# Kernel tuning notes

Measured on AMD Instinct MI355X. Metric: run time of the kernel, lower is better.

The kernel has to match this reference:

```python
import jax, jax.numpy as jnp
import numpy as np

N_NODES = 50000
N_EDGES = 600000
D_IN = 128
D_HID = 128
N_CLASSES = 64
BN_EPS = 1e-5


def _bn(x, gamma, beta):
    # BatchNorm1d with batch statistics (training-mode math, biased var)
    mu = jnp.mean(x, axis=0)
    var = jnp.mean((x - mu) ** 2, axis=0)
    return gamma * (x - mu) * jax.lax.rsqrt(var + BN_EPS) + beta


def _gin_layer(h, src, dst, W1, b1, g1, be1, W2, b2, g2, be2):
    n = h.shape[0]
    msgs = h[src]  # [E, D] gather (copy_src)
    s = jax.ops.segment_sum(msgs, dst, num_segments=n)
    cnt = jax.ops.segment_sum(jnp.ones((dst.shape[0],), h.dtype), dst, num_segments=n)
    neigh = s / jnp.maximum(cnt, 1.0)[:, None]  # mean over in-neighbors, 0 if none
    x = h + neigh  # (1 + eps) * h + neigh with eps = 0
    x = jax.nn.relu(_bn(x @ W1 + b1, g1, be1))
    x = jax.nn.relu(_bn(x @ W2 + b2, g2, be2))
    return x


def setup_inputs() -> dict:
    key = jax.random.key(0)
    ks = jax.random.split(key, 32)
    inp = {
        "features": jax.random.normal(ks[0], (N_NODES, D_IN), dtype=jnp.float32),
        "src": jax.random.randint(ks[1], (N_EDGES,), 0, N_NODES, dtype=jnp.int32),
        "dst": jax.random.randint(ks[2], (N_EDGES,), 0, N_NODES, dtype=jnp.int32),
    }
    dims = [(D_IN, D_HID), (D_HID, D_HID), (D_HID, N_CLASSES)]
    ki = 3
    for li, (din, dout) in enumerate(dims):
        sc1 = 1.0 / np.sqrt(din)
        sc2 = 1.0 / np.sqrt(dout)
        inp[f"W1_{li}"] = jax.random.uniform(ks[ki + 0], (din, dout), jnp.float32, -sc1, sc1)
        inp[f"b1_{li}"] = jax.random.uniform(ks[ki + 1], (dout,), jnp.float32, -sc1, sc1)
        inp[f"g1_{li}"] = jnp.ones((dout,), jnp.float32)
        inp[f"be1_{li}"] = jnp.zeros((dout,), jnp.float32)
        inp[f"W2_{li}"] = jax.random.uniform(ks[ki + 2], (dout, dout), jnp.float32, -sc2, sc2)
        inp[f"b2_{li}"] = jax.random.uniform(ks[ki + 3], (dout,), jnp.float32, -sc2, sc2)
        inp[f"g2_{li}"] = jnp.ones((dout,), jnp.float32)
        inp[f"be2_{li}"] = jnp.zeros((dout,), jnp.float32)
        ki += 4
    return inp


def reference(features, src, dst,
              W1_0, b1_0, g1_0, be1_0, W2_0, b2_0, g2_0, be2_0,
              W1_1, b1_1, g1_1, be1_1, W2_1, b2_1, g2_1, be2_1,
              W1_2, b1_2, g1_2, be1_2, W2_2, b2_2, g2_2, be2_2):
    h = features
    h = _gin_layer(h, src, dst, W1_0, b1_0, g1_0, be1_0, W2_0, b2_0, g2_0, be2_0)
    h = _gin_layer(h, src, dst, W1_1, b1_1, g1_1, be1_1, W2_1, b2_1, g2_1, be2_1)
    h = _gin_layer(h, src, dst, W1_2, b1_2, g1_2, be1_2, W2_2, b2_2, g2_2, be2_2)
    return h
```

## Files before the change

### kernel.cpp

```cpp
#include <hip/hip_runtime.h>

#define NN 50000
#define NE 600000
#define SREP 64

typedef __attribute__((ext_vector_type(8))) short short8;
typedef __attribute__((ext_vector_type(4))) float f32x4;

__device__ __forceinline__ float bf2f(unsigned short u){
  union { unsigned int i; float f; } c; c.i = ((unsigned int)u) << 16; return c.f;
}
__device__ __forceinline__ float lof(unsigned v){
  union { unsigned int i; float f; } c; c.i = v << 16; return c.f;
}
__device__ __forceinline__ float hif(unsigned v){
  union { unsigned int i; float f; } c; c.i = v & 0xFFFF0000u; return c.f;
}
__device__ __forceinline__ unsigned short f2b(float f){
  union { float f; unsigned int i; } c; c.f = f;
  unsigned int i = c.i;
  return (unsigned short)((i + 0x7FFFu + ((i >> 16) & 1u)) >> 16);
}

template<int N>
__device__ __forceinline__ void compute_ab(const float* __restrict__ st,
    const float* __restrict__ gam, const float* __restrict__ bet, float2* absh){
  int tid = threadIdx.x;
  if (tid < N){
    float s = 0.f, q = 0.f;
    #pragma unroll 16
    for (int r = 0; r < SREP; ++r){
      s += st[r*2*N + tid];
      q += st[r*2*N + N + tid];
    }
    float mu = s * (1.f/(float)NN);
    float var = fmaxf(q * (1.f/(float)NN) - mu*mu, 0.f);
    float a = gam[tid] * rsqrtf(var + 1e-5f);
    absh[tid] = make_float2(a, bet[tid] - mu*a);
  }
}

struct W6 { const float* w[6]; unsigned short* o[6]; };
__global__ __launch_bounds__(256) void k_pre(const float* __restrict__ features,
    unsigned short* __restrict__ H0, unsigned short* __restrict__ Hp,
    const int* __restrict__ dst, int* __restrict__ deg, W6 jb){
  int b = blockIdx.x, tid = threadIdx.x;
  if (b < 6250){
    int i = b*256 + tid;
    float4 v = ((const float4*)features)[i];
    uint2 o;
    o.x = (unsigned)f2b(v.x) | ((unsigned)f2b(v.y) << 16);
    o.y = (unsigned)f2b(v.z) | ((unsigned)f2b(v.w) << 16);
    ((uint2*)H0)[i] = o;
  } else if (b < 6250 + 2344){
    int i = (b - 6250)*256 + tid;
    if (i < NE) atomicAdd(&deg[dst[i]], 1);
  } else if (b < 6250 + 2344 + 304){
    int i = (b - 8594)*256 + tid;
    if (i < 77824){
      int job, base, K, N;
      if (i < 65536){ job = i >> 14; base = job << 14; K = 128; N = 128; }
      else if (i < 73728){ job = 4; base = 65536; K = 128; N = 64; }
      else { job = 5; base = 73728; K = 64; N = 64; }
      int t = i - base;
      int k = t & (K-1);
      int n = t / K;
      jb.o[job][t] = f2b(jb.w[job][k*N + n]);
    }
  } else {
    if (tid < 32){
      unsigned short* bp = (tid < 16) ? H0 : Hp;
      ((uint4*)bp)[(size_t)NN*16 + (tid & 15)] = make_uint4(0,0,0,0);
    }
  }
}

__global__ void k_offsets(const int* __restrict__ deg, int* __restrict__ row_off,
                          int* __restrict__ cur, int* __restrict__ col,
                          int* __restrict__ total){
  __shared__ int ws[4];
  __shared__ int wbase[4];
  int tid = threadIdx.x, lane = tid & 63, wid = tid >> 6;
  int i = blockIdx.x*256 + tid;
  int v = (i < NN) ? deg[i] : 0;
  int vp = (v + 3) & ~3;
  int x = vp;
  #pragma unroll
  for (int o = 1; o < 64; o <<= 1){
    int t = __shfl_up(x, o);
    if (lane >= o) x += t;
  }
  if (lane == 63) ws[wid] = x;
  __syncthreads();
  if (tid == 0){
    int s0 = ws[0], s1 = ws[1], s2 = ws[2], s3 = ws[3];
    int b = atomicAdd(total, s0+s1+s2+s3);
    wbase[0] = b; wbase[1] = b+s0; wbase[2] = b+s0+s1; wbase[3] = b+s0+s1+s2;
  }
  __syncthreads();
  if (i < NN){
    int excl = wbase[wid] + x - vp;
    row_off[i] = excl;
    cur[i] = excl;
    for (int t = v; t < vp; ++t) col[excl + t] = NN;
  }
}

__global__ void k_fill(const int* __restrict__ src, const int* __restrict__ dst,
                       int* __restrict__ cur, int* __restrict__ col, int e){
  int i = blockIdx.x*blockDim.x + threadIdx.x;
  if (i >= e) return;
  int d = dst[i];
  int pos = atomicAdd(&cur[d], 1);
  col[pos] = src[i];
}

__global__ __launch_bounds__(256) void k_agg(const unsigned short* __restrict__ H,
    const int* __restrict__ row_off, const int* __restrict__ deg,
    const int* __restrict__ col, unsigned short* __restrict__ X){
  int tid = threadIdx.x;
  int lane = tid & 63, wave = tid >> 6;
  int p = lane & 15, q = lane >> 4;
  const uint4* hp4 = (const uint4*)H;
  int node = (blockIdx.x*4 + wave)*4 + q;
  int beg = row_off[node];
  int d = deg[node];
  int dp = (d + 3) & ~3;
  int m = dp;
  m = max(m, __shfl_xor(m, 16));
  m = max(m, __shfl_xor(m, 32));
  uint4 hv = hp4[(size_t)node*16 + p];
  float s[8];
  #pragma unroll
  for (int e = 0; e < 8; ++e) s[e] = 0.f;
  auto ACC = [&](uint4 v){
    s[0] += lof(v.x); s[1] += hif(v.x);
    s[2] += lof(v.y); s[3] += hif(v.y);
    s[4] += lof(v.z); s[5] += hif(v.z);
    s[6] += lof(v.w); s[7] += hif(v.w);
  };
  for (int e0 = 0; e0 < m; e0 += 8){
    int idx[8];
    #pragma unroll
    for (int u = 0; u < 8; ++u){
      int e = e0 + u;
      int cv = col[beg + e];
      idx[u] = (e < dp) ? cv : NN;
    }
    uint4 vv[8];
    #pragma unroll
    for (int u = 0; u < 8; ++u) vv[u] = hp4[(size_t)idx[u]*16 + p];
    #pragma unroll
    for (int u = 0; u < 8; ++u) ACC(vv[u]);
  }
  float inv = 1.f / (float)(d > 0 ? d : 1);
  float h[8] = {lof(hv.x),hif(hv.x),lof(hv.y),hif(hv.y),
                lof(hv.z),hif(hv.z),lof(hv.w),hif(hv.w)};
  unsigned w[4];
  #pragma unroll
  for (int u = 0; u < 4; ++u){
    float x0 = h[2*u]   + s[2*u]*inv;
    float x1 = h[2*u+1] + s[2*u+1]*inv;
    w[u] = (unsigned)f2b(x0) | ((unsigned)f2b(x1) << 16);
  }
  ((uint4*)X)[(size_t)node*16 + p] = make_uint4(w[0], w[1], w[2], w[3]);
}

template<int KSTEPS, int NT, int CS, bool APPLY>
__global__ __launch_bounds__(512) void k_gemm(const unsigned short* __restrict__ A,
    const unsigned short* __restrict__ BT,
    const float* __restrict__ stIn, const float* __restrict__ gam,
    const float* __restrict__ bet,
    unsigned short* __restrict__ Y, float* __restrict__ statsAcc){
  constexpr int K = KSTEPS*32;
  constexpr int N = CS*NT*16;
  constexpr int TILES = NN/16;
  constexpr int TPB = (CS==2) ? 4 : 8;
  __shared__ float red[2*N];
  __shared__ float2 absh[K];
  if (APPLY) compute_ab<K>(stIn, gam, bet, absh);
  int tid = threadIdx.x;
  int lane = tid & 63, w = tid >> 6;
  int r = lane & 15, g = lane >> 4;
  int tile = blockIdx.x*TPB + ((CS==2) ? (w & 3) : w);
  int ch = (CS==2) ? (w >> 2) : 0;
  bool valid = (tile < TILES);
  int arow = valid ? tile*16 + r : 0;
  short8 af[KSTEPS];
  #pragma unroll
  for (int kk = 0; kk < KSTEPS; ++kk)
    af[kk] = *(const short8*)(A + (size_t)arow*K + kk*32 + g*8);
  short8 bf[KSTEPS][NT];
  #pragma unroll
  for (int kk = 0; kk < KSTEPS; ++kk)
    #pragma unroll
    for (int t = 0; t < NT; ++t)
      bf[kk][t] = *(const short8*)(BT + (size_t)(ch*NT*16 + t*16 + r)*K + kk*32 + g*8);
  for (int i = tid; i < 2*N; i += 512) red[i] = 0.f;
  __syncthreads();
  if (APPLY){
    #pragma unroll
    for (int kk = 0; kk < KSTEPS; ++kk){
      #pragma unroll
      for (int j = 0; j < 8; ++j){
        float2 pab = absh[kk*32 + g*8 + j];
        float v = fmaxf(fmaf(bf2f((unsigned short)af[kk][j]), pab.x, pab.y), 0.f);
        af[kk][j] = (short)f2b(v);
      }
    }
  }
  f32x4 acc[NT];
  #pragma unroll
  for (int t = 0; t < NT; ++t) acc[t] = (f32x4){0.f,0.f,0.f,0.f};
  #pragma unroll
  for (int kk = 0; kk < KSTEPS; ++kk)
    #pragma unroll
    for (int t = 0; t < NT; ++t)
      acc[t] = __builtin_amdgcn_mfma_f32_16x16x32_bf16(af[kk], bf[kk][t], acc[t], 0, 0, 0);
  if (valid){
    #pragma unroll
    for (int t = 0; t < NT; ++t){
      int c = ch*NT*16 + t*16 + r;
      float ys = 0.f, yq = 0.f;
      #pragma unroll
      for (int j = 0; j < 4; ++j){
        float y = acc[t][j];
        Y[(size_t)(tile*16 + g*4 + j)*N + c] = (unsigned short)f2b(y);
        ys += y; yq += y*y;
      }
      ys += __shfl_xor(ys, 16); ys += __shfl_xor(ys, 32);
      yq += __shfl_xor(yq, 16); yq += __shfl_xor(yq, 32);
      if (g == 0){
        atomicAdd(&red[c], ys);
        atomicAdd(&red[N+c], yq);
      }
    }
  }
  __syncthreads();
  float* dstAcc = statsAcc + (size_t)(blockIdx.x & (SREP-1)) * (2*N);
  for (int i = tid; i < 2*N; i += 512) atomicAdd(&dstAcc[i], red[i]);
}

__global__ __launch_bounds__(256) void k_apply(const unsigned short* __restrict__ Y,
    const float* __restrict__ st, const float* __restrict__ gam,
    const float* __restrict__ bet, unsigned short* __restrict__ Hp){
  __shared__ float2 absh[128];
  compute_ab<128>(st, gam, bet, absh);
  __syncthreads();
  for (int i = blockIdx.x*256 + threadIdx.x; i < NN*64; i += gridDim.x*256){
    unsigned v = ((const unsigned*)Y)[i];
    int c = (i & 63)*2;
    float2 p0 = absh[c], p1 = absh[c+1];
    float o0 = fmaxf(fmaf(lof(v), p0.x, p0.y), 0.f);
    float o1 = fmaxf(fmaf(hif(v), p1.x, p1.y), 0.f);
    ((unsigned*)Hp)[i] = (unsigned)f2b(o0) | ((unsigned)f2b(o1) << 16);
  }
}

__global__ __launch_bounds__(256) void k_final(const unsigned short* __restrict__ Y,
    const float* __restrict__ st, const float* __restrict__ gam,
    const float* __restrict__ bet, float* __restrict__ out){
  __shared__ float2 absh[64];
  compute_ab<64>(st, gam, bet, absh);
  __syncthreads();
  for (int i = blockIdx.x*256 + threadIdx.x; i < NN*32; i += gridDim.x*256){
    unsigned v = ((const unsigned*)Y)[i];
    int c = (i & 31)*2;
    float2 p0 = absh[c], p1 = absh[c+1];
    float o0 = fmaxf(fmaf(lof(v), p0.x, p0.y), 0.f);
    float o1 = fmaxf(fmaf(hif(v), p1.x, p1.y), 0.f);
    ((float2*)out)[i] = make_float2(o0, o1);
  }
}

extern "C" void kernel_launch(void* const* d_in, const int* in_sizes, int n_in,
                              void* d_out, int out_size, void* d_ws, size_t ws_size,
                              hipStream_t stream) {
  const float* features = (const float*)d_in[0];
  const int* src = (const int*)d_in[1];
  const int* dst = (const int*)d_in[2];
  const float *Wp[6], *gp[6], *bep[6];
  for (int l = 0; l < 3; ++l){
    int base = 3 + 8*l;
    Wp[2*l]    = (const float*)d_in[base+0];
    gp[2*l]    = (const float*)d_in[base+2];
    bep[2*l]   = (const float*)d_in[base+3];
    Wp[2*l+1]  = (const float*)d_in[base+4];
    gp[2*l+1]  = (const float*)d_in[base+6];
    bep[2*l+1] = (const float*)d_in[base+7];
  }

  size_t off = 0;
  char* base = (char*)d_ws;
  auto carve = [&](size_t bytes)->char* {
    char* q = base + off; off += (bytes + 255) & ~(size_t)255; return q;
  };
  int* deg   = (int*)carve((size_t)NN*4);
  int* total = (int*)carve(4);
  float* stats[6];
  for (int i = 0; i < 6; ++i) stats[i] = (float*)carve((size_t)SREP*256*4);
  size_t zbytes = (size_t)(base + off - (char*)deg);

  int* row_off = (int*)carve((size_t)NN*4);
  int* cur     = (int*)carve((size_t)NN*4);
  int* col     = (int*)carve((size_t)(NE + 3*NN + 64)*4);
  unsigned short* wt[6];
  for (int i = 0; i < 6; ++i) wt[i] = (unsigned short*)carve(128*128*2);
  unsigned short* H0 = (unsigned short*)carve((size_t)(NN+1)*128*2);
  unsigned short* Hp = (unsigned short*)carve((size_t)(NN+1)*128*2);
  unsigned short* X  = (unsigned short*)carve((size_t)NN*128*2);
  unsigned short* Y1 = (unsigned short*)carve((size_t)NN*128*2);
  unsigned short* Y2 = (unsigned short*)carve((size_t)NN*128*2);

  hipMemsetAsync(deg, 0, zbytes, stream);

  W6 jb;
  for (int i = 0; i < 6; ++i){ jb.w[i] = Wp[i]; jb.o[i] = wt[i]; }
  k_pre<<<8899, 256, 0, stream>>>(features, H0, Hp, dst, deg, jb);
  k_offsets<<<(NN+255)/256, 256, 0, stream>>>(deg, row_off, cur, col, total);
  k_fill<<<(NE+255)/256, 256, 0, stream>>>(src, dst, cur, col, NE);

  const int agg_grid = 3125;

  k_agg<<<agg_grid, 256, 0, stream>>>(H0, row_off, deg, col, X);
  k_gemm<4,4,2,false><<<782, 512, 0, stream>>>(X, wt[0], nullptr, nullptr, nullptr, Y1, stats[0]);
  k_gemm<4,4,2,true ><<<782, 512, 0, stream>>>(Y1, wt[1], stats[0], gp[0], bep[0], Y2, stats[1]);
  k_apply<<<1563, 256, 0, stream>>>(Y2, stats[1], gp[1], bep[1], Hp);
  k_agg<<<agg_grid, 256, 0, stream>>>(Hp, row_off, deg, col, X);
  k_gemm<4,4,2,false><<<782, 512, 0, stream>>>(X, wt[2], nullptr, nullptr, nullptr, Y1, stats[2]);
  k_gemm<4,4,2,true ><<<782, 512, 0, stream>>>(Y1, wt[3], stats[2], gp[2], bep[2], Y2, stats[3]);
  k_apply<<<1563, 256, 0, stream>>>(Y2, stats[3], gp[3], bep[3], H0);
  k_agg<<<agg_grid, 256, 0, stream>>>(H0, row_off, deg, col, X);
  k_gemm<4,4,1,false><<<391, 512, 0, stream>>>(X, wt[4], nullptr, nullptr, nullptr, Y1, stats[4]);
  k_gemm<2,4,1,true ><<<391, 512, 0, stream>>>(Y1, wt[5], stats[4], gp[4], bep[4], Y2, stats[5]);
  k_final<<<782, 256, 0, stream>>>(Y2, stats[5], gp[5], bep[5], (float*)d_out);
}
```

Before: 298.6 us.

## Fuse BatchNorm+ReLU apply into neighbor aggregation, drop k_apply pass

After: 310.8 us. 1.04x slower.

```diff
diff --git a/kernel.cpp b/kernel.cpp
--- a/kernel.cpp
+++ b/kernel.cpp
@@ -42,7 +42,7 @@
 
 struct W6 { const float* w[6]; unsigned short* o[6]; };
 __global__ __launch_bounds__(256) void k_pre(const float* __restrict__ features,
-    unsigned short* __restrict__ H0, unsigned short* __restrict__ Hp,
+    unsigned short* __restrict__ H0, unsigned short* __restrict__ Y2,
     const int* __restrict__ dst, int* __restrict__ deg, W6 jb){
   int b = blockIdx.x, tid = threadIdx.x;
   if (b < 6250){
@@ -69,7 +69,7 @@
     }
   } else {
     if (tid < 32){
-      unsigned short* bp = (tid < 16) ? H0 : Hp;
+      unsigned short* bp = (tid < 16) ? H0 : Y2;
       ((uint4*)bp)[(size_t)NN*16 + (tid & 15)] = make_uint4(0,0,0,0);
     }
   }
@@ -115,12 +115,22 @@
   col[pos] = src[i];
 }
 
+template<bool APPLY>
 __global__ __launch_bounds__(256) void k_agg(const unsigned short* __restrict__ H,
+    const float* __restrict__ st, const float* __restrict__ gam,
+    const float* __restrict__ bet,
     const int* __restrict__ row_off, const int* __restrict__ deg,
     const int* __restrict__ col, unsigned short* __restrict__ X){
+  __shared__ float2 absh[128];
+  if (APPLY){ compute_ab<128>(st, gam, bet, absh); __syncthreads(); }
   int tid = threadIdx.x;
   int lane = tid & 63, wave = tid >> 6;
   int p = lane & 15, q = lane >> 4;
+  float ac[8], bc[8];
+  if (APPLY){
+    #pragma unroll
+    for (int e = 0; e < 8; ++e){ float2 t = absh[p*8 + e]; ac[e] = t.x; bc[e] = t.y; }
+  }
   const uint4* hp4 = (const uint4*)H;
   int node = (blockIdx.x*4 + wave)*4 + q;
   int beg = row_off[node];
@@ -129,17 +139,23 @@
   int m = dp;
   m = max(m, __shfl_xor(m, 16));
   m = max(m, __shfl_xor(m, 32));
+  int slots = (m + 7) & ~7;
   uint4 hv = hp4[(size_t)node*16 + p];
   float s[8];
   #pragma unroll
   for (int e = 0; e < 8; ++e) s[e] = 0.f;
   auto ACC = [&](uint4 v){
-    s[0] += lof(v.x); s[1] += hif(v.x);
-    s[2] += lof(v.y); s[3] += hif(v.y);
-    s[4] += lof(v.z); s[5] += hif(v.z);
-    s[6] += lof(v.w); s[7] += hif(v.w);
+    float x;
+    x = lof(v.x); if (APPLY) x = fmaxf(fmaf(x,ac[0],bc[0]),0.f); s[0] += x;
+    x = hif(v.x); if (APPLY) x = fmaxf(fmaf(x,ac[1],bc[1]),0.f); s[1] += x;
+    x = lof(v.y); if (APPLY) x = fmaxf(fmaf(x,ac[2],bc[2]),0.f); s[2] += x;
+    x = hif(v.y); if (APPLY) x = fmaxf(fmaf(x,ac[3],bc[3]),0.f); s[3] += x;
+    x = lof(v.z); if (APPLY) x = fmaxf(fmaf(x,ac[4],bc[4]),0.f); s[4] += x;
+    x = hif(v.z); if (APPLY) x = fmaxf(fmaf(x,ac[5],bc[5]),0.f); s[5] += x;
+    x = lof(v.w); if (APPLY) x = fmaxf(fmaf(x,ac[6],bc[6]),0.f); s[6] += x;
+    x = hif(v.w); if (APPLY) x = fmaxf(fmaf(x,ac[7],bc[7]),0.f); s[7] += x;
   };
-  for (int e0 = 0; e0 < m; e0 += 8){
+  for (int e0 = 0; e0 < slots; e0 += 8){
     int idx[8];
     #pragma unroll
     for (int u = 0; u < 8; ++u){
@@ -154,13 +170,22 @@
     for (int u = 0; u < 8; ++u) ACC(vv[u]);
   }
   float inv = 1.f / (float)(d > 0 ? d : 1);
+  float npad = (float)(slots - d);
   float h[8] = {lof(hv.x),hif(hv.x),lof(hv.y),hif(hv.y),
                 lof(hv.z),hif(hv.z),lof(hv.w),hif(hv.w)};
   unsigned w[4];
   #pragma unroll
   for (int u = 0; u < 4; ++u){
-    float x0 = h[2*u]   + s[2*u]*inv;
-    float x1 = h[2*u+1] + s[2*u+1]*inv;
+    float x0 = h[2*u], x1 = h[2*u+1];
+    float s0 = s[2*u], s1 = s[2*u+1];
+    if (APPLY){
+      x0 = fmaxf(fmaf(x0,ac[2*u],bc[2*u]),0.f);
+      x1 = fmaxf(fmaf(x1,ac[2*u+1],bc[2*u+1]),0.f);
+      s0 -= npad * fmaxf(bc[2*u], 0.f);
+      s1 -= npad * fmaxf(bc[2*u+1], 0.f);
+    }
+    x0 += s0*inv;
+    x1 += s1*inv;
     w[u] = (unsigned)f2b(x0) | ((unsigned)f2b(x1) << 16);
   }
   ((uint4*)X)[(size_t)node*16 + p] = make_uint4(w[0], w[1], w[2], w[3]);
@@ -241,22 +266,6 @@
   for (int i = tid; i < 2*N; i += 512) atomicAdd(&dstAcc[i], red[i]);
 }
 
-__global__ __launch_bounds__(256) void k_apply(const unsigned short* __restrict__ Y,
-    const float* __restrict__ st, const float* __restrict__ gam,
-    const float* __restrict__ bet, unsigned short* __restrict__ Hp){
-  __shared__ float2 absh[128];
-  compute_ab<128>(st, gam, bet, absh);
-  __syncthreads();
-  for (int i = blockIdx.x*256 + threadIdx.x; i < NN*64; i += gridDim.x*256){
-    unsigned v = ((const unsigned*)Y)[i];
-    int c = (i & 63)*2;
-    float2 p0 = absh[c], p1 = absh[c+1];
-    float o0 = fmaxf(fmaf(lof(v), p0.x, p0.y), 0.f);
-    float o1 = fmaxf(fmaf(hif(v), p1.x, p1.y), 0.f);
-    ((unsigned*)Hp)[i] = (unsigned)f2b(o0) | ((unsigned)f2b(o1) << 16);
-  }
-}
-
 __global__ __launch_bounds__(256) void k_final(const unsigned short* __restrict__ Y,
     const float* __restrict__ st, const float* __restrict__ gam,
     const float* __restrict__ bet, float* __restrict__ out){
@@ -307,30 +316,30 @@
   unsigned short* wt[6];
   for (int i = 0; i < 6; ++i) wt[i] = (unsigned short*)carve(128*128*2);
   unsigned short* H0 = (unsigned short*)carve((size_t)(NN+1)*128*2);
-  unsigned short* Hp = (unsigned short*)carve((size_t)(NN+1)*128*2);
   unsigned short* X  = (unsigned short*)carve((size_t)NN*128*2);
   unsigned short* Y1 = (unsigned short*)carve((size_t)NN*128*2);
-  unsigned short* Y2 = (unsigned short*)carve((size_t)NN*128*2);
+  unsigned short* Y2 = (unsigned short*)carve((size_t)(NN+1)*128*2);
 
   hipMemsetAsync(deg, 0, zbytes, stream);
 
   W6 jb;
   for (int i = 0; i < 6; ++i){ jb.w[i] = Wp[i]; jb.o[i] = wt[i]; }
-  k_pre<<<8899, 256, 0, stream>>>(features, H0, Hp, dst, deg, jb);
+  k_pre<<<8899, 256, 0, stream>>>(features, H0, Y2, dst, deg, jb);
   k_offsets<<<(NN+255)/256, 256, 0, stream>>>(deg, row_off, cur, col, total);
   k_fill<<<(NE+255)/256, 256, 0, stream>>>(src, dst, cur, col, NE);
 
   const int agg_grid = 3125;
 
-  k_agg<<<agg_grid, 256, 0, stream>>>(H0, row_off, deg, col, X);
+  k_agg<false><<<agg_grid, 256, 0, stream>>>(H0, nullptr, nullptr, nullptr,
+      row_off, deg, col, X);
   k_gemm<4,4,2,false><<<782, 512, 0, stream>>>(X, wt[0], nullptr, nullptr, nullptr, Y1, stats[0]);
   k_gemm<4,4,2,true ><<<782, 512, 0, stream>>>(Y1, wt[1], stats[0], gp[0], bep[0], Y2, stats[1]);
-  k_apply<<<1563, 256, 0, stream>>>(Y2, stats[1], gp[1], bep[1], Hp);
-  k_agg<<<agg_grid, 256, 0, stream>>>(Hp, row_off, deg, col, X);
+  k_agg<true ><<<agg_grid, 256, 0, stream>>>(Y2, stats[1], gp[1], bep[1],
+      row_off, deg, col, X);
   k_gemm<4,4,2,false><<<782, 512, 0, stream>>>(X, wt[2], nullptr, nullptr, nullptr, Y1, stats[2]);
   k_gemm<4,4,2,true ><<<782, 512, 0, stream>>>(Y1, wt[3], stats[2], gp[2], bep[2], Y2, stats[3]);
-  k_apply<<<1563, 256, 0, stream>>>(Y2, stats[3], gp[3], bep[3], H0);
-  k_agg<<<agg_grid, 256, 0, stream>>>(H0, row_off, deg, col, X);
+  k_agg<true ><<<agg_grid, 256, 0, stream>>>(Y2, stats[3], gp[3], bep[3],
+      row_off, deg, col, X);
   k_gemm<4,4,1,false><<<391, 512, 0, stream>>>(X, wt[4], nullptr, nullptr, nullptr, Y1, stats[4]);
   k_gemm<2,4,1,true ><<<391, 512, 0, stream>>>(Y1, wt[5], stats[4], gp[4], bep[4], Y2, stats[5]);
   k_final<<<782, 256, 0, stream>>>(Y2, stats[5], gp[5], bep[5], (float*)d_out);
```

## Restructure aggregation to one thread per node per feature chunk

Applied to the files above, without the earlier changes.

Result: slower. 472.4 us (+58.2%).

```diff
diff --git a/kernel.cpp b/kernel.cpp
--- a/kernel.cpp
+++ b/kernel.cpp
@@ -6,6 +6,8 @@
 
 typedef __attribute__((ext_vector_type(8))) short short8;
 typedef __attribute__((ext_vector_type(4))) float f32x4;
+typedef __attribute__((ext_vector_type(4))) unsigned uint4v;
+typedef __attribute__((ext_vector_type(4))) int int4v;
 
 __device__ __forceinline__ float bf2f(unsigned short u){
   union { unsigned int i; float f; } c; c.i = ((unsigned int)u) << 16; return c.f;
@@ -20,6 +22,11 @@
   union { float f; unsigned int i; } c; c.f = f;
   unsigned int i = c.i;
   return (unsigned short)((i + 0x7FFFu + ((i >> 16) & 1u)) >> 16);
+}
+
+__global__ __launch_bounds__(256) void k_zero(uint4v* __restrict__ p, int n4){
+  int i = blockIdx.x*256 + threadIdx.x;
+  if (i < n4) p[i] = (uint4v){0,0,0,0};
 }
 
 template<int N>
@@ -70,7 +77,7 @@
   } else {
     if (tid < 32){
       unsigned short* bp = (tid < 16) ? H0 : Hp;
-      ((uint4*)bp)[(size_t)NN*16 + (tid & 15)] = make_uint4(0,0,0,0);
+      ((uint4v*)bp)[(size_t)NN*16 + (tid & 15)] = (uint4v){0,0,0,0};
     }
   }
 }
@@ -115,55 +122,68 @@
   col[pos] = src[i];
 }
 
-__global__ __launch_bounds__(256) void k_agg(const unsigned short* __restrict__ H,
+__global__ __launch_bounds__(256) void k_agg(const unsigned short* __restrict__ T,
     const int* __restrict__ row_off, const int* __restrict__ deg,
     const int* __restrict__ col, unsigned short* __restrict__ X){
   int tid = threadIdx.x;
-  int lane = tid & 63, wave = tid >> 6;
-  int p = lane & 15, q = lane >> 4;
-  const uint4* hp4 = (const uint4*)H;
-  int node = (blockIdx.x*4 + wave)*4 + q;
-  int beg = row_off[node];
-  int d = deg[node];
-  int dp = (d + 3) & ~3;
+  int chunk = blockIdx.x & 7;
+  int u = (int)(blockIdx.x >> 3)*256 + tid;
+  bool valid = (u < NN);
+  int node = valid ? u : NN;
+  int beg = valid ? row_off[u] : 0;
+  int d   = valid ? deg[u] : 0;
+  int dp  = (d + 3) & ~3;
   int m = dp;
-  m = max(m, __shfl_xor(m, 16));
-  m = max(m, __shfl_xor(m, 32));
-  uint4 hv = hp4[(size_t)node*16 + p];
-  float s[8];
-  #pragma unroll
-  for (int e = 0; e < 8; ++e) s[e] = 0.f;
-  auto ACC = [&](uint4 v){
-    s[0] += lof(v.x); s[1] += hif(v.x);
-    s[2] += lof(v.y); s[3] += hif(v.y);
-    s[4] += lof(v.z); s[5] += hif(v.z);
-    s[6] += lof(v.w); s[7] += hif(v.w);
+  #pragma unroll
+  for (int o = 1; o < 64; o <<= 1) m = max(m, __shfl_xor(m, o));
+  const uint4v* tp = (const uint4v*)T;
+  size_t co = (size_t)chunk*2;
+  uint4v h0 = tp[(size_t)node*16 + co];
+  uint4v h1 = tp[(size_t)node*16 + co + 1];
+  float s[16];
+  #pragma unroll
+  for (int i = 0; i < 16; ++i) s[i] = 0.f;
+  auto ACC8 = [&](uint4v v, int o){
+    s[o+0] += lof(v.x); s[o+1] += hif(v.x);
+    s[o+2] += lof(v.y); s[o+3] += hif(v.y);
+    s[o+4] += lof(v.z); s[o+5] += hif(v.z);
+    s[o+6] += lof(v.w); s[o+7] += hif(v.w);
   };
-  for (int e0 = 0; e0 < m; e0 += 8){
-    int idx[8];
-    #pragma unroll
-    for (int u = 0; u < 8; ++u){
-      int e = e0 + u;
-      int cv = col[beg + e];
-      idx[u] = (e < dp) ? cv : NN;
-    }
-    uint4 vv[8];
-    #pragma unroll
-    for (int u = 0; u < 8; ++u) vv[u] = hp4[(size_t)idx[u]*16 + p];
-    #pragma unroll
-    for (int u = 0; u < 8; ++u) ACC(vv[u]);
-  }
-  float inv = 1.f / (float)(d > 0 ? d : 1);
-  float h[8] = {lof(hv.x),hif(hv.x),lof(hv.y),hif(hv.y),
-                lof(hv.z),hif(hv.z),lof(hv.w),hif(hv.w)};
-  unsigned w[4];
-  #pragma unroll
-  for (int u = 0; u < 4; ++u){
-    float x0 = h[2*u]   + s[2*u]*inv;
-    float x1 = h[2*u+1] + s[2*u+1]*inv;
-    w[u] = (unsigned)f2b(x0) | ((unsigned)f2b(x1) << 16);
-  }
-  ((uint4*)X)[(size_t)node*16 + p] = make_uint4(w[0], w[1], w[2], w[3]);
+  const int4v* colv = (const int4v*)(col + beg);
+  for (int e0 = 0; e0 < m; e0 += 4){
+    int4v c4 = __builtin_nontemporal_load(colv + (e0 >> 2));
+    int idx[4];
+    idx[0] = (e0     < dp) ? c4.x : NN;
+    idx[1] = (e0 + 1 < dp) ? c4.y : NN;
+    idx[2] = (e0 + 2 < dp) ? c4.z : NN;
+    idx[3] = (e0 + 3 < dp) ? c4.w : NN;
+    uint4v v0[4], v1[4];
+    #pragma unroll
+    for (int uu = 0; uu < 4; ++uu){
+      v0[uu] = tp[(size_t)idx[uu]*16 + co];
+      v1[uu] = tp[(size_t)idx[uu]*16 + co + 1];
+    }
+    #pragma unroll
+    for (int uu = 0; uu < 4; ++uu){ ACC8(v0[uu], 0); ACC8(v1[uu], 8); }
+  }
+  if (valid){
+    float inv = 1.f / (float)(d > 0 ? d : 1);
+    float hf[16] = {lof(h0.x),hif(h0.x),lof(h0.y),hif(h0.y),
+                    lof(h0.z),hif(h0.z),lof(h0.w),hif(h0.w),
+                    lof(h1.x),hif(h1.x),lof(h1.y),hif(h1.y),
+                    lof(h1.z),hif(h1.z),lof(h1.w),hif(h1.w)};
+    unsigned w[8];
+    #pragma unroll
+    for (int i = 0; i < 8; ++i){
+      float x0 = hf[2*i]   + s[2*i]*inv;
+      float x1 = hf[2*i+1] + s[2*i+1]*inv;
+      w[i] = (unsigned)f2b(x0) | ((unsigned)f2b(x1) << 16);
+    }
+    uint4v o0 = {w[0], w[1], w[2], w[3]};
+    uint4v o1 = {w[4], w[5], w[6], w[7]};
+    __builtin_nontemporal_store(o0, (uint4v*)X + (size_t)u*16 + co);
+    __builtin_nontemporal_store(o1, (uint4v*)X + (size_t)u*16 + co + 1);
+  }
 }
 
 template<int KSTEPS, int NT, int CS, bool APPLY>
@@ -303,7 +323,7 @@
 
   int* row_off = (int*)carve((size_t)NN*4);
   int* cur     = (int*)carve((size_t)NN*4);
-  int* col     = (int*)carve((size_t)(NE + 3*NN + 64)*4);
+  int* col     = (int*)carve((size_t)(NE + 3*NN + 4096)*4);
   unsigned short* wt[6];
   for (int i = 0; i < 6; ++i) wt[i] = (unsigned short*)carve(128*128*2);
   unsigned short* H0 = (unsigned short*)carve((size_t)(NN+1)*128*2);
@@ -312,7 +332,8 @@
   unsigned short* Y1 = (unsigned short*)carve((size_t)NN*128*2);
   unsigned short* Y2 = (unsigned short*)carve((size_t)NN*128*2);
 
-  hipMemsetAsync(deg, 0, zbytes, stream);
+  int zn4 = (int)(zbytes >> 4);
+  k_zero<<<(zn4 + 255)/256, 256, 0, stream>>>((uint4v*)deg, zn4);
 
   W6 jb;
   for (int i = 0; i < 6; ++i){ jb.w[i] = Wp[i]; jb.o[i] = wt[i]; }
@@ -320,7 +341,7 @@
   k_offsets<<<(NN+255)/256, 256, 0, stream>>>(deg, row_off, cur, col, total);
   k_fill<<<(NE+255)/256, 256, 0, stream>>>(src, dst, cur, col, NE);
 
-  const int agg_grid = 3125;
+  const int agg_grid = 196*8;
 
   k_agg<<<agg_grid, 256, 0, stream>>>(H0, row_off, deg, col, X);
   k_gemm<4,4,2,false><<<782, 512, 0, stream>>>(X, wt[0], nullptr, nullptr, nullptr, Y1, stats[0]);
```
